# Kernel tuning notes

Measured on AMD Instinct MI355X. Metric: run time of the kernel, lower is better.

Reference implementation:

```python
import jax, jax.numpy as jnp
import numpy as np

TWO_PI = 2.0 * np.pi
NUM_STEPS = 16
DT = 0.1
K_STRENGTH = 1.0
TAU = 1.0


def setup_inputs() -> dict:
    key = jax.random.key(0)
    k1, k2, k3 = jax.random.split(key, 3)
    B, N, D = 8, 2048, 128
    initial_state = jax.random.uniform(k1, (B, N), dtype=jnp.float32) * TWO_PI
    embeddings = jax.random.normal(k2, (B, N, D), dtype=jnp.float32)
    omega = jax.random.normal(k3, (N,), dtype=jnp.float32) * 0.1
    return {"initial_state": initial_state, "embeddings": embeddings, "omega": omega}


def _build_coupling(embeddings):
    # Lorentz/geodesic coupling: K = exp(-acosh(clamp(-<u,v>_L, 1+eps)) / tau)
    t = embeddings[..., :1]            # [B,N,1] time component
    s = embeddings[..., 1:]            # [B,N,D-1] spatial components
    spatial_inner = jnp.einsum("bnd,bmd->bnm", s, s)          # [B,N,N]
    lorentz_inner = spatial_inner - t * jnp.swapaxes(t, 1, 2)  # [B,N,N]
    arg = jnp.maximum(-lorentz_inner, 1.0 + 1e-7)
    d_L = jnp.arccosh(arg)
    coupling = jnp.exp(-d_L / (TAU + 1e-6))
    return jnp.clip(coupling, 0.0, 1.0)


def reference(initial_state, embeddings, omega):
    B, N = initial_state.shape
    coupling = _build_coupling(embeddings)  # [B,N,N]

    def step(theta, _):
        # all-pairs phase difference theta_i - theta_j: [B,N,N]
        phase_diff = theta[:, :, None] - theta[:, None, :]
        coupling_sum = jnp.sum(coupling * jnp.sin(phase_diff), axis=2)  # [B,N]
        dtheta = omega[None, :] + (K_STRENGTH / N) * coupling_sum
        theta = jnp.fmod(theta + DT * dtheta, TWO_PI)
        return theta, None

    theta, _ = jax.lax.scan(step, initial_state, None, length=NUM_STEPS)
    return theta
```

## Files before the change

### kernel.cpp

```cpp
#include <hip/hip_runtime.h>
#include <hip/hip_bf16.h>

#define BB 8
#define NN 2048
#define DD 128
#define NSTEPS 16
#define DT_F 0.1f
#define TWO_PI_F 6.283185307179586f

typedef short short8 __attribute__((ext_vector_type(8)));
typedef float floatx4 __attribute__((ext_vector_type(4)));

__global__ void split_kernel(const float* __restrict__ e,
                             __hip_bfloat16* __restrict__ hi,
                             __hip_bfloat16* __restrict__ lo) {
    int i = blockIdx.x * 256 + threadIdx.x;
    float x = e[i];
    __hip_bfloat16 h = __float2bfloat16(x);
    hi[i] = h;
    lo[i] = __float2bfloat16(x - __bfloat162float(h));
}

#define LDP 136

__launch_bounds__(256, 2)
__global__ void coupling_kernel(const __hip_bfloat16* __restrict__ Ehi,
                                const __hip_bfloat16* __restrict__ Elo,
                                __hip_bfloat16* __restrict__ C) {
    __shared__ __hip_bfloat16 Ah[64 * LDP];
    __shared__ __hip_bfloat16 Al[64 * LDP];
    __shared__ __hip_bfloat16 Bh[64 * LDP];
    __shared__ __hip_bfloat16 Bl[64 * LDP];

    const int b  = blockIdx.z;
    const int n0 = blockIdx.y * 64;
    const int m0 = blockIdx.x * 64;
    const int tid = threadIdx.x;

    const __hip_bfloat16* aHsrc = Ehi + ((size_t)b * NN + n0) * DD;
    const __hip_bfloat16* aLsrc = Elo + ((size_t)b * NN + n0) * DD;
    const __hip_bfloat16* bHsrc = Ehi + ((size_t)b * NN + m0) * DD;
    const __hip_bfloat16* bLsrc = Elo + ((size_t)b * NN + m0) * DD;

    #pragma unroll
    for (int i = 0; i < 4; ++i) {
        int c   = tid + 256 * i;
        int row = c >> 4;
        int col = (c & 15) * 8;
        *(uint4*)(Ah + row * LDP + col) = *(const uint4*)(aHsrc + row * DD + col);
        *(uint4*)(Al + row * LDP + col) = *(const uint4*)(aLsrc + row * DD + col);
        *(uint4*)(Bh + row * LDP + col) = *(const uint4*)(bHsrc + row * DD + col);
        *(uint4*)(Bl + row * LDP + col) = *(const uint4*)(bLsrc + row * DD + col);
    }
    __syncthreads();

    const int wave = tid >> 6;
    const int lane = tid & 63;
    const int l16  = lane & 15;
    const int quad = lane >> 4;

    floatx4 acc[4] = {floatx4{0,0,0,0}, floatx4{0,0,0,0},
                      floatx4{0,0,0,0}, floatx4{0,0,0,0}};

    const int arow = wave * 16 + l16;
    #pragma unroll
    for (int kt = 0; kt < 4; ++kt) {
        const int ko = kt * 32 + quad * 8;
        short8 ah = *(const short8*)(Ah + arow * LDP + ko);
        short8 al = *(const short8*)(Al + arow * LDP + ko);
        #pragma unroll
        for (int c = 0; c < 4; ++c) {
            const int brow = c * 16 + l16;
            short8 bh = *(const short8*)(Bh + brow * LDP + ko);
            short8 bl = *(const short8*)(Bl + brow * LDP + ko);
            acc[c] = __builtin_amdgcn_mfma_f32_16x16x32_bf16(ah, bh, acc[c], 0, 0, 0);
            acc[c] = __builtin_amdgcn_mfma_f32_16x16x32_bf16(ah, bl, acc[c], 0, 0, 0);
            acc[c] = __builtin_amdgcn_mfma_f32_16x16x32_bf16(al, bh, acc[c], 0, 0, 0);
        }
    }

    float tn2[4];
    #pragma unroll
    for (int i = 0; i < 4; ++i) {
        int r = wave * 16 + quad * 4 + i;
        tn2[i] = 2.0f * (__bfloat162float(Ah[r * LDP]) + __bfloat162float(Al[r * LDP]));
    }
    #pragma unroll
    for (int c = 0; c < 4; ++c) {
        int br = c * 16 + l16;
        float tm = __bfloat162float(Bh[br * LDP]) + __bfloat162float(Bl[br * LDP]);
        size_t base = ((size_t)b * NN + n0 + wave * 16 + quad * 4) * (size_t)NN
                      + m0 + c * 16 + l16;
        #pragma unroll
        for (int i = 0; i < 4; ++i) {
            float g   = acc[c][i];
            float arg = fmaxf(fmaf(tn2[i], tm, -g), 1.0f + 1e-7f);
            float s   = sqrtf(fmaf(arg, arg, -1.0f));
            float cp  = __builtin_amdgcn_rcpf(arg + s);
            C[base + (size_t)i * NN] = __float2bfloat16(fminf(cp, 1.0f));
        }
    }
}

__launch_bounds__(256, 3)
__global__ void step_kernel(const __hip_bfloat16* __restrict__ C,
                            const float* __restrict__ theta_in,
                            float* __restrict__ theta_out,
                            const float* __restrict__ omega) {
    __shared__ float2 cs[NN];
    const int tid = threadIdx.x;
    const int b   = blockIdx.x >> 7;
    const int rb  = blockIdx.x & 127;
    const float* th_b = theta_in + b * NN;

    #pragma unroll
    for (int i = 0; i < 8; ++i) {
        int m = tid + 256 * i;
        float sv, cv;
        sincosf(th_b[m], &sv, &cv);
        cs[m] = make_float2(cv, sv);
    }
    __syncthreads();

    const int lane = tid & 63;
    const int wave = tid >> 6;

    float cc[32], ss[32];
    #pragma unroll
    for (int j = 0; j < 4; ++j) {
        #pragma unroll
        for (int i = 0; i < 8; ++i) {
            float2 v = cs[j * 512 + lane * 8 + i];
            cc[j * 8 + i] = v.x;
            ss[j * 8 + i] = v.y;
        }
    }

    const int row0 = rb * 16 + wave * 4;
    const __hip_bfloat16* Cb = C + ((size_t)b * NN + row0) * (size_t)NN + lane * 8;

    uint4 v[4][4];
    #pragma unroll
    for (int q = 0; q < 4; ++q)
        #pragma unroll
        for (int j = 0; j < 4; ++j)
            v[q][j] = *(const uint4*)(Cb + (size_t)q * NN + j * 512);

    float ac[4], as[4];
    #pragma unroll
    for (int q = 0; q < 4; ++q) {
        float a0 = 0.f, a1 = 0.f, s0 = 0.f, s1 = 0.f;
        #pragma unroll
        for (int j = 0; j < 4; ++j) {
            unsigned u[4] = {v[q][j].x, v[q][j].y, v[q][j].z, v[q][j].w};
            #pragma unroll
            for (int k = 0; k < 4; ++k) {
                float f0 = __uint_as_float(u[k] << 16);
                float f1 = __uint_as_float(u[k] & 0xffff0000u);
                int idx = j * 8 + 2 * k;
                a0 = fmaf(f0, cc[idx],     a0);
                s0 = fmaf(f0, ss[idx],     s0);
                a1 = fmaf(f1, cc[idx + 1], a1);
                s1 = fmaf(f1, ss[idx + 1], s1);
            }
        }
        ac[q] = a0 + a1;
        as[q] = s0 + s1;
    }

    #pragma unroll
    for (int q = 0; q < 4; ++q) {
        #pragma unroll
        for (int off = 32; off >= 1; off >>= 1) {
            ac[q] += __shfl_xor(ac[q], off, 64);
            as[q] += __shfl_xor(as[q], off, 64);
        }
    }

    if (lane < 4) {
        int q = lane;
        int n = row0 + q;
        float2 csn = cs[n];
        float sum  = csn.y * ac[q] - csn.x * as[q];
        float th   = th_b[n];
        float dth  = omega[n] + (1.0f / NN) * sum;
        theta_out[b * NN + n] = fmodf(th + DT_F * dth, TWO_PI_F);
    }
}

extern "C" void kernel_launch(void* const* d_in, const int* in_sizes, int n_in,
                              void* d_out, int out_size, void* d_ws, size_t ws_size,
                              hipStream_t stream) {
    const float* theta0 = (const float*)d_in[0];
    const float* emb    = (const float*)d_in[1];
    const float* omega  = (const float*)d_in[2];
    float* out = (float*)d_out;

    char* ws = (char*)d_ws;
    __hip_bfloat16* C   = (__hip_bfloat16*)ws;
    __hip_bfloat16* Ehi = (__hip_bfloat16*)(ws + 67108864);
    __hip_bfloat16* Elo = (__hip_bfloat16*)(ws + 71303168);
    float* tA = (float*)(ws + 75497472);
    float* tB = (float*)(ws + 75563008);

    split_kernel<<<(BB * NN * DD) / 256, 256, 0, stream>>>(emb, Ehi, Elo);

    dim3 g1(NN / 64, NN / 64, BB);
    coupling_kernel<<<g1, 256, 0, stream>>>(Ehi, Elo, C);

    const float* tin = theta0;
    for (int s = 0; s < NSTEPS; ++s) {
        float* tout = (s == NSTEPS - 1) ? out : ((s & 1) ? tB : tA);
        step_kernel<<<dim3(BB * (NN / 16)), 256, 0, stream>>>(C, tin, tout, omega);
        tin = tout;
    }
}
```

Baseline: 386.9 us.

## Stream coupling rows into LDS with triple-buffered async loads in step kernel

Each wave now handles 8 rows instead of 4. Rows of the coupling matrix are fetched with global_load_lds into a per-wave triple buffer, and manual vmcnt waits let the next row's load overlap the current row's FMAs. The grid is halved and launch bounds drop to 2 blocks per SM because of the extra LDS. sincosf is also replaced with the faster __sincosf intrinsic, which is less accurate. This risks lower occupancy and relies on hand-placed waitcnt encodings being correct.

```diff
diff --git a/kernel.cpp b/kernel.cpp
--- a/kernel.cpp
+++ b/kernel.cpp
@@ -10,6 +10,8 @@
 
 typedef short short8 __attribute__((ext_vector_type(8)));
 typedef float floatx4 __attribute__((ext_vector_type(4)));
+
+#define WAITVM(N) __builtin_amdgcn_s_waitcnt(0xF70 | (N))
 
 __global__ void split_kernel(const float* __restrict__ e,
                              __hip_bfloat16* __restrict__ hi,
@@ -102,28 +104,75 @@
     }
 }
 
-__launch_bounds__(256, 3)
+
+__device__ __forceinline__ void issue_row(const __hip_bfloat16* gsrc,
+                                          __hip_bfloat16* lds_row) {
+    #pragma unroll
+    for (int k = 0; k < 4; ++k) {
+        __builtin_amdgcn_global_load_lds(
+            (const __attribute__((address_space(1))) unsigned int*)(gsrc + k * 512),
+            (__attribute__((address_space(3))) unsigned int*)(lds_row + k * 512),
+            16, 0, 0);
+    }
+}
+
+__device__ __forceinline__ void consume_row(const __hip_bfloat16* lrow, int lane,
+                                            const float (&cc)[32], const float (&ss)[32],
+                                            float& outc, float& outs) {
+    float a0 = 0.f, a1 = 0.f, s0 = 0.f, s1 = 0.f;
+    #pragma unroll
+    for (int j = 0; j < 4; ++j) {
+        uint4 v = *(const uint4*)(lrow + j * 512 + lane * 8);
+        unsigned u[4] = {v.x, v.y, v.z, v.w};
+        #pragma unroll
+        for (int k = 0; k < 4; ++k) {
+            float f0 = __uint_as_float(u[k] << 16);
+            float f1 = __uint_as_float(u[k] & 0xffff0000u);
+            int idx = j * 8 + 2 * k;
+            a0 = fmaf(f0, cc[idx],     a0);
+            s0 = fmaf(f0, ss[idx],     s0);
+            a1 = fmaf(f1, cc[idx + 1], a1);
+            s1 = fmaf(f1, ss[idx + 1], s1);
+        }
+    }
+    outc = a0 + a1;
+    outs = s0 + s1;
+}
+
+__launch_bounds__(256, 2)
 __global__ void step_kernel(const __hip_bfloat16* __restrict__ C,
                             const float* __restrict__ theta_in,
                             float* __restrict__ theta_out,
                             const float* __restrict__ omega) {
     __shared__ float2 cs[NN];
+    __shared__ __align__(16) __hip_bfloat16 cbuf[4][3][2048];
+
     const int tid = threadIdx.x;
-    const int b   = blockIdx.x >> 7;
-    const int rb  = blockIdx.x & 127;
+    const int b   = blockIdx.x >> 6;
+    const int rg  = blockIdx.x & 63;
     const float* th_b = theta_in + b * NN;
+
+    const int lane = tid & 63;
+    const int wave = tid >> 6;
+    const int row0 = rg * 32 + wave * 8;
+
+    const size_t NNs = NN;
+    const __hip_bfloat16* Cw = C + ((size_t)b * NN + row0) * NNs + lane * 8;
+    __hip_bfloat16* lb = &cbuf[wave][0][0];
 
     #pragma unroll
     for (int i = 0; i < 8; ++i) {
         int m = tid + 256 * i;
         float sv, cv;
-        sincosf(th_b[m], &sv, &cv);
+        __sincosf(th_b[m], &sv, &cv);
         cs[m] = make_float2(cv, sv);
     }
+
+    issue_row(Cw,            lb);
+    issue_row(Cw + NNs,      lb + 2048);
+    issue_row(Cw + 2 * NNs,  lb + 4096);
+
     __syncthreads();
-
-    const int lane = tid & 63;
-    const int wave = tid >> 6;
 
     float cc[32], ss[32];
     #pragma unroll
@@ -136,55 +185,45 @@
         }
     }
 
-    const int row0 = rb * 16 + wave * 4;
-    const __hip_bfloat16* Cb = C + ((size_t)b * NN + row0) * (size_t)NN + lane * 8;
-
-    uint4 v[4][4];
-    #pragma unroll
-    for (int q = 0; q < 4; ++q)
-        #pragma unroll
-        for (int j = 0; j < 4; ++j)
-            v[q][j] = *(const uint4*)(Cb + (size_t)q * NN + j * 512);
-
-    float ac[4], as[4];
-    #pragma unroll
-    for (int q = 0; q < 4; ++q) {
-        float a0 = 0.f, a1 = 0.f, s0 = 0.f, s1 = 0.f;
-        #pragma unroll
-        for (int j = 0; j < 4; ++j) {
-            unsigned u[4] = {v[q][j].x, v[q][j].y, v[q][j].z, v[q][j].w};
-            #pragma unroll
-            for (int k = 0; k < 4; ++k) {
-                float f0 = __uint_as_float(u[k] << 16);
-                float f1 = __uint_as_float(u[k] & 0xffff0000u);
-                int idx = j * 8 + 2 * k;
-                a0 = fmaf(f0, cc[idx],     a0);
-                s0 = fmaf(f0, ss[idx],     s0);
-                a1 = fmaf(f1, cc[idx + 1], a1);
-                s1 = fmaf(f1, ss[idx + 1], s1);
-            }
-        }
-        ac[q] = a0 + a1;
-        as[q] = s0 + s1;
-    }
-
-    #pragma unroll
-    for (int q = 0; q < 4; ++q) {
+    float sumc[8], sums[8];
+    consume_row(lb,        lane, cc, ss, sumc[0], sums[0]);
+    issue_row(Cw + 3 * NNs, lb);
+    consume_row(lb + 2048, lane, cc, ss, sumc[1], sums[1]);
+    issue_row(Cw + 4 * NNs, lb + 2048);
+    consume_row(lb + 4096, lane, cc, ss, sumc[2], sums[2]);
+    issue_row(Cw + 5 * NNs, lb + 4096);
+    WAITVM(8);
+    consume_row(lb,        lane, cc, ss, sumc[3], sums[3]);
+    issue_row(Cw + 6 * NNs, lb);
+    WAITVM(8);
+    consume_row(lb + 2048, lane, cc, ss, sumc[4], sums[4]);
+    issue_row(Cw + 7 * NNs, lb + 2048);
+    WAITVM(8);
+    consume_row(lb + 4096, lane, cc, ss, sumc[5], sums[5]);
+    WAITVM(4);
+    consume_row(lb,        lane, cc, ss, sumc[6], sums[6]);
+    WAITVM(0);
+    consume_row(lb + 2048, lane, cc, ss, sumc[7], sums[7]);
+
+    #pragma unroll
+    for (int r = 0; r < 8; ++r) {
         #pragma unroll
         for (int off = 32; off >= 1; off >>= 1) {
-            ac[q] += __shfl_xor(ac[q], off, 64);
-            as[q] += __shfl_xor(as[q], off, 64);
-        }
-    }
-
-    if (lane < 4) {
-        int q = lane;
-        int n = row0 + q;
-        float2 csn = cs[n];
-        float sum  = csn.y * ac[q] - csn.x * as[q];
-        float th   = th_b[n];
-        float dth  = omega[n] + (1.0f / NN) * sum;
-        theta_out[b * NN + n] = fmodf(th + DT_F * dth, TWO_PI_F);
+            sumc[r] += __shfl_xor(sumc[r], off, 64);
+            sums[r] += __shfl_xor(sums[r], off, 64);
+        }
+    }
+
+    #pragma unroll
+    for (int r = 0; r < 8; ++r) {
+        if (lane == r) {
+            int n = row0 + r;
+            float2 csn = cs[n];
+            float sum  = csn.y * sumc[r] - csn.x * sums[r];
+            float th   = th_b[n];
+            float dth  = omega[n] + (1.0f / NN) * sum;
+            theta_out[b * NN + n] = fmodf(th + DT_F * dth, TWO_PI_F);
+        }
     }
 }
 
@@ -211,7 +250,7 @@
     const float* tin = theta0;
     for (int s = 0; s < NSTEPS; ++s) {
         float* tout = (s == NSTEPS - 1) ? out : ((s & 1) ? tB : tA);
-        step_kernel<<<dim3(BB * (NN / 16)), 256, 0, stream>>>(C, tin, tout, omega);
+        step_kernel<<<dim3(BB * (NN / 32)), 256, 0, stream>>>(C, tin, tout, omega);
         tin = tout;
     }
 }
```

Result: faster. 369.0 us (-4.6%).
